# Kernel optimization log

Hardware: AMD Instinct MI355X
Metric: run time of the kernel (lower is better)

Reference implementation:

```python
import jax, jax.numpy as jnp
import numpy as np
import math

SCALES = (1, 2, 4, 8)


def interp1d(x, L_out):
    """F.interpolate(mode='linear', align_corners=False) along last axis."""
    L_in = x.shape[-1]
    if L_in == L_out:
        return x
    scale = L_in / L_out
    src = (jnp.arange(L_out, dtype=jnp.float32) + 0.5) * scale - 0.5
    src = jnp.clip(src, 0.0, float(L_in - 1))
    i0 = jnp.floor(src).astype(jnp.int32)
    i1 = jnp.minimum(i0 + 1, L_in - 1)
    w1 = (src - i0.astype(jnp.float32)).astype(x.dtype)
    return x[..., i0] * (1.0 - w1) + x[..., i1] * w1


def setup_inputs() -> dict:
    key = jax.random.key(0)
    ks = jax.random.split(key, 5)
    B, H, S, D = 2, 16, 1024, 64
    query = jax.random.normal(ks[0], (B, H, S, D), jnp.float32)
    k = jax.random.normal(ks[1], (B, H, S, D), jnp.float32)
    v = jax.random.normal(ks[2], (B, H, S, D), jnp.float32)
    # 4 per-scale Linear(head_dim, head_dim): W[i] is [out, in] (torch layout), b[i] is [out]
    W = jax.random.normal(ks[3], (len(SCALES), D, D), jnp.float32) * (1.0 / np.sqrt(D))
    b = jax.random.normal(ks[4], (len(SCALES), D), jnp.float32) * 0.01
    return {"query": query, "key": k, "value": v, "W": W, "b": b}


def reference(query, key, value, W, b):
    B, H, S, D = query.shape
    inv_sqrt_d = 1.0 / math.sqrt(D)
    outs, probs_all = [], []
    for i, s in enumerate(SCALES):
        if s > 1:
            # avg_pool1d(kernel=stride=s) over the sequence axis
            pk = key.reshape(B, H, S // s, s, D).mean(axis=3)
            pv = value.reshape(B, H, S // s, s, D).mean(axis=3)
        else:
            pk, pv = key, value
        # per-scale linear projection of pooled keys (torch Linear: x @ W.T + b)
        proj = jnp.einsum('bhkd,ed->bhke', pk, W[i]) + b[i]
        scores = jnp.einsum('bhqd,bhkd->bhqk', query, proj) * inv_sqrt_d
        probs = jax.nn.softmax(scores, axis=-1)  # [B,H,S,S//s]
        if s > 1:
            # upsample attn probs along key axis, and pooled values along seq axis
            probs = interp1d(probs, S)                               # [B,H,S,S]
            pv = jnp.swapaxes(interp1d(jnp.swapaxes(pv, -1, -2), S), -1, -2)  # [B,H,S,D]
        outs.append(jnp.einsum('bhqk,bhkd->bhqd', probs, pv))
        probs_all.append(probs)
    combined_output = jnp.stack(outs).mean(axis=0)
    combined_attention = jnp.stack(probs_all).mean(axis=0)
    return combined_output, combined_attention
```

## Files before the change

kernel.cpp:

```cpp
#include <hip/hip_runtime.h>

#define S_LEN 1024
#define DH 64
#define NBH 32
#define CROWS 1920
#define HEAD_K (CROWS * DH)
#define NCHUNK (HEAD_K / 8)
#define ATTN_OFF (NBH * S_LEN * DH)
#define PSTR 1928

typedef __attribute__((ext_vector_type(8))) short bf8_t;
typedef __attribute__((ext_vector_type(4))) float f32x4_t;

__device__ __forceinline__ unsigned short f2bf(float x) {
  unsigned u = __float_as_uint(x);
  u += 0x7fffu + ((u >> 16) & 1u);
  return (unsigned short)(u >> 16);
}
__device__ __forceinline__ float bf2f(unsigned short h) {
  return __uint_as_float(((unsigned)h) << 16);
}

template<int SI>
__device__ __forceinline__ void prep_body(
    const float* __restrict__ key, const float* __restrict__ value,
    const float* __restrict__ W, const float* __restrict__ b,
    unsigned short* __restrict__ projB, unsigned short* __restrict__ mpvB,
    const int bh, const int jt, const int t,
    float* __restrict__ pkK, float* __restrict__ pkV, float* __restrict__ coefs)
{
  constexpr int   s    = 1 << SI;
  constexpr int   L    = 1024 >> SI;
  constexpr int   off  = (SI == 0) ? 0 : (SI == 1) ? 1024 : (SI == 2) ? 1536 : 1792;
  constexpr float invs = 1.0f / (float)s;
  const int j0 = jt << 6;

  const float* Kp = key + bh * (S_LEN * DH);
  const float* Vp = value + bh * (S_LEN * DH);

  #pragma unroll
  for (int it = 0; it < 4; it++) {
    const int i = it * 256 + t;
    const int j = i >> 4, d4 = (i & 15) << 2;
    const float* src = Kp + (j0 + j) * s * DH + d4;
    float4 a = {0.f, 0.f, 0.f, 0.f};
    #pragma unroll
    for (int f = 0; f < s; f++) {
      const float4 kv = *(const float4*)(src + f * DH);
      a.x += kv.x; a.y += kv.y; a.z += kv.z; a.w += kv.w;
    }
    a.x *= invs; a.y *= invs; a.z *= invs; a.w *= invs;
    *(float4*)&pkK[j * 68 + d4] = a;
  }

  #pragma unroll
  for (int it = 0; it < 5; it++) {
    const int i = it * 256 + t;
    if (i < 1088) {
      const int hj = i >> 4, d4 = (i & 15) << 2;
      const int jg = min(max(j0 - 2 + hj, 0), L - 1);
      const float* src = Vp + jg * s * DH + d4;
      float4 a = {0.f, 0.f, 0.f, 0.f};
      #pragma unroll
      for (int f = 0; f < s; f++) {
        const float4 vv = *(const float4*)(src + f * DH);
        a.x += vv.x; a.y += vv.y; a.z += vv.z; a.w += vv.w;
      }
      a.x *= invs; a.y *= invs; a.z *= invs; a.w *= invs;
      *(float4*)&pkV[hj * 68 + d4] = a;
    }
  }

  if (t < 64) {
    const int j = j0 + t;
    float cm = 0.f, cc = 0.f, cp = 0.f;
    const int klo = max(0, (j - 1) * s);
    const int khi = min(S_LEN - 1, (j + 2) * s);
    for (int kf = klo; kf <= khi; kf++) {
      float srcp = ((float)kf + 0.5f) * invs - 0.5f;
      srcp = fminf(fmaxf(srcp, 0.f), (float)(L - 1));
      const int i0 = (int)floorf(srcp);
      const int i1 = min(i0 + 1, L - 1);
      const float w = srcp - (float)i0;
      float u = 0.f;
      if (i0 == j) u += 1.f - w;
      if (i1 == j) u += w;
      if (u != 0.f) {
        const float g0 = u * (1.f - w), g1 = u * w;
        if (i0 == j) cc += g0; else cm += g0;
        if (i1 == j) cc += g1; else cp += g1;
      }
    }
    coefs[t * 4 + 0] = cm; coefs[t * 4 + 1] = cc; coefs[t * 4 + 2] = cp;
  }
  __syncthreads();

  {
    const int j  = t & 63;
    const int e0 = __builtin_amdgcn_readfirstlane((t >> 6) << 4);
    const float* Wp = W + SI * 4096;
    float acc[16];
    #pragma unroll
    for (int ee = 0; ee < 16; ee++) acc[ee] = b[SI * 64 + e0 + ee];
    #pragma unroll
    for (int dq = 0; dq < 16; dq++) {
      const float4 p4 = *(const float4*)&pkK[j * 68 + dq * 4];
      #pragma unroll
      for (int ee = 0; ee < 16; ee++) {
        const float4 w4 = *(const float4*)&Wp[(e0 + ee) * 64 + dq * 4];
        acc[ee] += p4.x * w4.x + p4.y * w4.y + p4.z * w4.z + p4.w * w4.w;
      }
    }
    const int ktg0 = (off + j0) >> 4;
    const int ktl  = j >> 4;
    #pragma unroll
    for (int h = 0; h < 2; h++) {
      const int e0p = e0 + h * 8;
      const int ln  = (((e0p >> 3) & 3) << 4) | (j & 15);
      bf8_t v;
      #pragma unroll
      for (int jj = 0; jj < 8; jj++) v[jj] = (short)f2bf(acc[h * 8 + jj]);
      ((bf8_t*)projB)[bh * NCHUNK + ((ktg0 + ktl) * 2 + (e0p >> 5)) * 64 + ln] = v;
    }
  }

  const int kbg0 = (off + j0) >> 5;
  #pragma unroll
  for (int cc2 = 0; cc2 < 2; cc2++) {
    const int c   = cc2 * 256 + t;
    const int kbl = c >> 8;
    const int nt  = (c >> 6) & 3;
    const int ln  = c & 63;
    const int d   = nt * 16 + (ln & 15);
    const int r0  = kbl * 32 + ((ln >> 4) & 3) * 8;
    bf8_t v;
    #pragma unroll
    for (int jj = 0; jj < 8; jj++) {
      const int rl = r0 + jj;
      const float val = coefs[rl * 4 + 0] * pkV[(rl + 1) * 68 + d] +
                        coefs[rl * 4 + 1] * pkV[(rl + 2) * 68 + d] +
                        coefs[rl * 4 + 2] * pkV[(rl + 3) * 68 + d];
      v[jj] = (short)f2bf(val);
    }
    ((bf8_t*)mpvB)[bh * NCHUNK + ((kbg0 + kbl) * 4 + nt) * 64 + ln] = v;
  }
}

__global__ __launch_bounds__(256, 4) void prep_kernel(
    const float* __restrict__ key, const float* __restrict__ value,
    const float* __restrict__ W, const float* __restrict__ b,
    unsigned short* __restrict__ projB, unsigned short* __restrict__ mpvB)
{
  __shared__ __align__(16) float pkK[64 * 68];
  __shared__ __align__(16) float pkV[68 * 68];
  __shared__ float coefs[64 * 4];
  const int t = threadIdx.x;
  const int bid = blockIdx.x;
  const int bh = bid / 30;
  const int tt = bid % 30;
  if (tt < 16)
    prep_body<0>(key, value, W, b, projB, mpvB, bh, tt, t, pkK, pkV, coefs);
  else if (tt < 24)
    prep_body<1>(key, value, W, b, projB, mpvB, bh, tt - 16, t, pkK, pkV, coefs);
  else if (tt < 28)
    prep_body<2>(key, value, W, b, projB, mpvB, bh, tt - 24, t, pkK, pkV, coefs);
  else
    prep_body<3>(key, value, W, b, projB, mpvB, bh, tt - 28, t, pkK, pkV, coefs);
}

__global__ __launch_bounds__(256, 2) void fused_attn_kernel(
    const float* __restrict__ query, const unsigned short* __restrict__ projB,
    const unsigned short* __restrict__ mpvB, float* __restrict__ out)
{
  __shared__ __align__(16) unsigned short prbf[16 * PSTR];
  const int t    = threadIdx.x;
  const int bid  = blockIdx.x;
  const int xcd  = bid & 7;
  const int slot = bid >> 3;
  const int bh   = xcd * 4 + (slot >> 6);
  const int qt   = slot & 63;
  const int q0   = qt << 4;
  const int wave = t >> 6;
  const int lane = t & 63;
  const int quad = lane >> 4;
  const int n16  = lane & 15;

  bf8_t af0, af1;
  {
    const float* qrow = query + bh * (S_LEN * DH) + (q0 + n16) * DH;
    const float4 a0 = *(const float4*)(qrow + quad * 8);
    const float4 a1 = *(const float4*)(qrow + quad * 8 + 4);
    const float4 a2 = *(const float4*)(qrow + 32 + quad * 8);
    const float4 a3 = *(const float4*)(qrow + 32 + quad * 8 + 4);
    af0[0] = (short)f2bf(a0.x); af0[1] = (short)f2bf(a0.y);
    af0[2] = (short)f2bf(a0.z); af0[3] = (short)f2bf(a0.w);
    af0[4] = (short)f2bf(a1.x); af0[5] = (short)f2bf(a1.y);
    af0[6] = (short)f2bf(a1.z); af0[7] = (short)f2bf(a1.w);
    af1[0] = (short)f2bf(a2.x); af1[1] = (short)f2bf(a2.y);
    af1[2] = (short)f2bf(a2.z); af1[3] = (short)f2bf(a2.w);
    af1[4] = (short)f2bf(a3.x); af1[5] = (short)f2bf(a3.y);
    af1[6] = (short)f2bf(a3.z); af1[7] = (short)f2bf(a3.w);
  }

  {
    const bf8_t* pB = (const bf8_t*)projB + bh * NCHUNK;
    bf8_t pb0 = pB[(wave * 2 + 0) * 64 + lane];
    bf8_t pb1 = pB[(wave * 2 + 1) * 64 + lane];
    for (int kt = wave; kt < 120; kt += 4) {
      const int ktn = min(kt + 4, 119);
      const bf8_t nb0 = pB[(ktn * 2 + 0) * 64 + lane];
      const bf8_t nb1 = pB[(ktn * 2 + 1) * 64 + lane];
      f32x4_t c = {0.f, 0.f, 0.f, 0.f};
      c = __builtin_amdgcn_mfma_f32_16x16x32_bf16(af0, pb0, c, 0, 0, 0);
      c = __builtin_amdgcn_mfma_f32_16x16x32_bf16(af1, pb1, c, 0, 0, 0);
      const int col = kt * 16 + n16;
      #pragma unroll
      for (int i = 0; i < 4; i++)
        prbf[(quad * 4 + i) * PSTR + col] = f2bf(c[i] * 0.125f);
      pb0 = nb0; pb1 = nb1;
    }
  }
  __syncthreads();

  {
    const int rr = t >> 4;
    const int g  = t & 15;
    unsigned short* prr = prbf + rr * PSTR;
    #pragma unroll
    for (int si = 0; si < 4; si++) {
      const int L   = 1024 >> si;
      const int off = (si == 0) ? 0 : (si == 1) ? 1024 : (si == 2) ? 1536 : 1792;
      const int nch = L >> 2;
      float m = -1e30f;
      for (int ch = g; ch < nch; ch += 16) {
        const ushort4 u = *(const ushort4*)(prr + off + ch * 4);
        m = fmaxf(m, fmaxf(fmaxf(bf2f(u.x), bf2f(u.y)),
                           fmaxf(bf2f(u.z), bf2f(u.w))));
      }
      #pragma unroll
      for (int dlt = 8; dlt >= 1; dlt >>= 1) m = fmaxf(m, __shfl_xor(m, dlt));
      float ssum = 0.f;
      for (int ch = g; ch < nch; ch += 16) {
        ushort4 u = *(const ushort4*)(prr + off + ch * 4);
        const float e0 = __expf(bf2f(u.x) - m);
        const float e1 = __expf(bf2f(u.y) - m);
        const float e2 = __expf(bf2f(u.z) - m);
        const float e3 = __expf(bf2f(u.w) - m);
        ssum += (e0 + e1) + (e2 + e3);
        u.x = f2bf(e0); u.y = f2bf(e1); u.z = f2bf(e2); u.w = f2bf(e3);
        *(ushort4*)(prr + off + ch * 4) = u;
      }
      #pragma unroll
      for (int dlt = 8; dlt >= 1; dlt >>= 1) ssum += __shfl_xor(ssum, dlt);
      const float inv = 1.0f / ssum;
      for (int ch = g; ch < nch; ch += 16) {
        ushort4 u = *(const ushort4*)(prr + off + ch * 4);
        u.x = f2bf(bf2f(u.x) * inv); u.y = f2bf(bf2f(u.y) * inv);
        u.z = f2bf(bf2f(u.z) * inv); u.w = f2bf(bf2f(u.w) * inv);
        *(ushort4*)(prr + off + ch * 4) = u;
      }
    }
  }
  __syncthreads();

  {
    const bf8_t* pM = (const bf8_t*)mpvB + bh * NCHUNK;
    f32x4_t acc = {0.f, 0.f, 0.f, 0.f};
    bf8_t bb0 = pM[(0 * 4 + wave) * 64 + lane];
    bf8_t bb1 = pM[(1 * 4 + wave) * 64 + lane];
    for (int kb = 0; kb < 60; kb++) {
      const int kbn = min(kb + 2, 59);
      const bf8_t bbn = pM[(kbn * 4 + wave) * 64 + lane];
      const bf8_t a = *(const bf8_t*)(prbf + n16 * PSTR + kb * 32 + quad * 8);
      acc = __builtin_amdgcn_mfma_f32_16x16x32_bf16(a, bb0, acc, 0, 0, 0);
      bb0 = bb1; bb1 = bbn;
    }
    float* ob = out + bh * (S_LEN * DH) + q0 * DH;
    #pragma unroll
    for (int i = 0; i < 4; i++)
      __builtin_nontemporal_store(acc[i] * 0.25f,
                                  &ob[(quad * 4 + i) * DH + wave * 16 + n16]);
  }

  float* ab = out + ATTN_OFF + (size_t)bh * (S_LEN * S_LEN) + (size_t)q0 * S_LEN;
  for (int rep = 0; rep < 16; rep++) {
    const int idx = rep * 256 + t;
    const int rr  = idx >> 8;
    const int k0  = (idx & 255) << 2;
    const unsigned short* p2 = prbf + rr * PSTR;
    const ushort4 bs = *(const ushort4*)(p2 + k0);
    float res[4] = {bf2f(bs.x), bf2f(bs.y), bf2f(bs.z), bf2f(bs.w)};
    #pragma unroll
    for (int si = 1; si < 4; si++) {
      const int   L     = 1024 >> si;
      const int   off2  = (si == 1) ? 1024 : (si == 2) ? 1536 : 1792;
      const float inv_s = (si == 1) ? 0.5f : (si == 2) ? 0.25f : 0.125f;
      #pragma unroll
      for (int kk = 0; kk < 4; kk++) {
        float srcp = ((float)(k0 + kk) + 0.5f) * inv_s - 0.5f;
        srcp = fminf(fmaxf(srcp, 0.f), (float)(L - 1));
        const int i0 = (int)floorf(srcp);
        const int i1 = min(i0 + 1, L - 1);
        const float w = srcp - (float)i0;
        res[kk] += (1.f - w) * bf2f(p2[off2 + i0]) + w * bf2f(p2[off2 + i1]);
      }
    }
    f32x4_t o4;
    o4[0] = res[0] * 0.25f; o4[1] = res[1] * 0.25f;
    o4[2] = res[2] * 0.25f; o4[3] = res[3] * 0.25f;
    __builtin_nontemporal_store(o4, (f32x4_t*)(ab + (size_t)idx * 4));
  }
}

extern "C" void kernel_launch(void* const* d_in, const int* in_sizes, int n_in,
                              void* d_out, int out_size, void* d_ws, size_t ws_size,
                              hipStream_t stream) {
  (void)in_sizes; (void)n_in; (void)out_size; (void)ws_size;
  const float* query = (const float*)d_in[0];
  const float* key   = (const float*)d_in[1];
  const float* value = (const float*)d_in[2];
  const float* W     = (const float*)d_in[3];
  const float* b     = (const float*)d_in[4];
  float* out = (float*)d_out;

  unsigned short* projB = (unsigned short*)d_ws;
  unsigned short* mpvB  = projB + (size_t)NBH * HEAD_K;

  prep_kernel<<<NBH * 30, 256, 0, stream>>>(key, value, W, b, projB, mpvB);
  fused_attn_kernel<<<NBH * 64, 256, 0, stream>>>(query, projB, mpvB, out);
}
```

Measured before the change: 294.9 us.

## Defer softmax normalization into PV accumulation and attention-map output

Removes the third LDS pass that multiplied each bf16 probability by 1/sum. The per-row, per-scale reciprocal is stored in shared memory instead. The PV MFMA loop is split into four accumulators, one per scale segment, and each is scaled by its reciprocal at the end. The interpolation indices and weights are hoisted out of the 16-row loop, since each thread now owns fixed columns. Skipping the rounding step slightly changes numerics and adds register pressure from the precomputed index arrays.

```diff
diff --git a/kernel.cpp b/kernel.cpp
--- a/kernel.cpp
+++ b/kernel.cpp
@@ -173,6 +173,7 @@
     const unsigned short* __restrict__ mpvB, float* __restrict__ out)
 {
   __shared__ __align__(16) unsigned short prbf[16 * PSTR];
+  __shared__ float sInv[16 * 4];
   const int t    = threadIdx.x;
   const int bid  = blockIdx.x;
   const int xcd  = bid & 7;
@@ -252,44 +253,46 @@
       }
       #pragma unroll
       for (int dlt = 8; dlt >= 1; dlt >>= 1) ssum += __shfl_xor(ssum, dlt);
-      const float inv = 1.0f / ssum;
-      for (int ch = g; ch < nch; ch += 16) {
-        ushort4 u = *(const ushort4*)(prr + off + ch * 4);
-        u.x = f2bf(bf2f(u.x) * inv); u.y = f2bf(bf2f(u.y) * inv);
-        u.z = f2bf(bf2f(u.z) * inv); u.w = f2bf(bf2f(u.w) * inv);
-        *(ushort4*)(prr + off + ch * 4) = u;
-      }
+      if (g == 0) sInv[rr * 4 + si] = 1.0f / ssum;
     }
   }
   __syncthreads();
 
   {
     const bf8_t* pM = (const bf8_t*)mpvB + bh * NCHUNK;
-    f32x4_t acc = {0.f, 0.f, 0.f, 0.f};
+    f32x4_t s0 = {0.f, 0.f, 0.f, 0.f}, s1 = s0, s2 = s0, s3 = s0;
     bf8_t bb0 = pM[(0 * 4 + wave) * 64 + lane];
     bf8_t bb1 = pM[(1 * 4 + wave) * 64 + lane];
-    for (int kb = 0; kb < 60; kb++) {
-      const int kbn = min(kb + 2, 59);
-      const bf8_t bbn = pM[(kbn * 4 + wave) * 64 + lane];
-      const bf8_t a = *(const bf8_t*)(prbf + n16 * PSTR + kb * 32 + quad * 8);
-      acc = __builtin_amdgcn_mfma_f32_16x16x32_bf16(a, bb0, acc, 0, 0, 0);
-      bb0 = bb1; bb1 = bbn;
-    }
+    #define P3_STEP(ACC, KB)                                                   \
+      {                                                                        \
+        const int kbn = min((KB) + 2, 59);                                     \
+        const bf8_t bbn = pM[(kbn * 4 + wave) * 64 + lane];                    \
+        const bf8_t a =                                                        \
+            *(const bf8_t*)(prbf + n16 * PSTR + (KB) * 32 + quad * 8);         \
+        ACC = __builtin_amdgcn_mfma_f32_16x16x32_bf16(a, bb0, ACC, 0, 0, 0);   \
+        bb0 = bb1; bb1 = bbn;                                                  \
+      }
+    for (int kb = 0; kb < 32; kb++)  P3_STEP(s0, kb)
+    for (int kb = 32; kb < 48; kb++) P3_STEP(s1, kb)
+    for (int kb = 48; kb < 56; kb++) P3_STEP(s2, kb)
+    for (int kb = 56; kb < 60; kb++) P3_STEP(s3, kb)
+    #undef P3_STEP
     float* ob = out + bh * (S_LEN * DH) + q0 * DH;
     #pragma unroll
-    for (int i = 0; i < 4; i++)
-      __builtin_nontemporal_store(acc[i] * 0.25f,
-                                  &ob[(quad * 4 + i) * DH + wave * 16 + n16]);
-  }
-
-  float* ab = out + ATTN_OFF + (size_t)bh * (S_LEN * S_LEN) + (size_t)q0 * S_LEN;
-  for (int rep = 0; rep < 16; rep++) {
-    const int idx = rep * 256 + t;
-    const int rr  = idx >> 8;
-    const int k0  = (idx & 255) << 2;
-    const unsigned short* p2 = prbf + rr * PSTR;
-    const ushort4 bs = *(const ushort4*)(p2 + k0);
-    float res[4] = {bf2f(bs.x), bf2f(bs.y), bf2f(bs.z), bf2f(bs.w)};
+    for (int i = 0; i < 4; i++) {
+      const int row = quad * 4 + i;
+      const float val =
+          0.25f * (s0[i] * sInv[row * 4 + 0] + s1[i] * sInv[row * 4 + 1] +
+                   s2[i] * sInv[row * 4 + 2] + s3[i] * sInv[row * 4 + 3]);
+      __builtin_nontemporal_store(val, &ob[row * DH + wave * 16 + n16]);
+    }
+  }
+
+  {
+    float* ab = out + ATTN_OFF + (size_t)bh * (S_LEN * S_LEN) + (size_t)q0 * S_LEN;
+    const int k0 = t << 2;
+    int   io0[3][4], io1[3][4];
+    float wgt[3][4];
     #pragma unroll
     for (int si = 1; si < 4; si++) {
       const int   L     = 1024 >> si;
@@ -300,15 +303,36 @@
         float srcp = ((float)(k0 + kk) + 0.5f) * inv_s - 0.5f;
         srcp = fminf(fmaxf(srcp, 0.f), (float)(L - 1));
         const int i0 = (int)floorf(srcp);
-        const int i1 = min(i0 + 1, L - 1);
-        const float w = srcp - (float)i0;
-        res[kk] += (1.f - w) * bf2f(p2[off2 + i0]) + w * bf2f(p2[off2 + i1]);
-      }
-    }
-    f32x4_t o4;
-    o4[0] = res[0] * 0.25f; o4[1] = res[1] * 0.25f;
-    o4[2] = res[2] * 0.25f; o4[3] = res[3] * 0.25f;
-    __builtin_nontemporal_store(o4, (f32x4_t*)(ab + (size_t)idx * 4));
+        io0[si - 1][kk] = off2 + i0;
+        io1[si - 1][kk] = off2 + min(i0 + 1, L - 1);
+        wgt[si - 1][kk] = srcp - (float)i0;
+      }
+    }
+    for (int rr = 0; rr < 16; rr++) {
+      const unsigned short* p2 = prbf + rr * PSTR;
+      const float iv0 = sInv[rr * 4 + 0];
+      const float iv1 = sInv[rr * 4 + 1];
+      const float iv2 = sInv[rr * 4 + 2];
+      const float iv3 = sInv[rr * 4 + 3];
+      const ushort4 bs = *(const ushort4*)(p2 + k0);
+      float res[4] = {bf2f(bs.x) * iv0, bf2f(bs.y) * iv0,
+                      bf2f(bs.z) * iv0, bf2f(bs.w) * iv0};
+      #pragma unroll
+      for (int si = 1; si < 4; si++) {
+        const float ivs = (si == 1) ? iv1 : (si == 2) ? iv2 : iv3;
+        #pragma unroll
+        for (int kk = 0; kk < 4; kk++) {
+          const float w  = wgt[si - 1][kk];
+          const float e0 = bf2f(p2[io0[si - 1][kk]]);
+          const float e1 = bf2f(p2[io1[si - 1][kk]]);
+          res[kk] += ivs * (e0 + w * (e1 - e0));
+        }
+      }
+      f32x4_t o4;
+      o4[0] = res[0] * 0.25f; o4[1] = res[1] * 0.25f;
+      o4[2] = res[2] * 0.25f; o4[3] = res[3] * 0.25f;
+      __builtin_nontemporal_store(o4, (f32x4_t*)(ab + rr * 1024 + k0));
+    }
   }
 }
 
```

After: 286.5 us. 1.03x faster.
